# Performance work log

Measured on AMD Instinct MI355X. Metric: run time of the kernel, lower is better.

The kernel has to match this reference:

```python
import jax, jax.numpy as jnp
import numpy as np

B, C, V, L = 32, 32, 1024, 13  # batch, channels, nodes, seq_len
SUPPORT_LEN, ORDER = 3, 2
C_IN_TOTAL = (ORDER * SUPPORT_LEN + 1) * C  # 224
C_OUT = 64


def setup_inputs() -> dict:
    key = jax.random.key(0)
    ks = jax.random.split(key, 6)
    x = jax.random.normal(ks[0], (B, C, V, L), dtype=jnp.float32)
    # row-normalized random adjacencies (dense diffusion matrices)
    def adj(k):
        a = jax.random.uniform(k, (V, V), dtype=jnp.float32)
        return a / jnp.sum(a, axis=1, keepdims=True)
    A0, A1, A2 = adj(ks[1]), adj(ks[2]), adj(ks[3])
    W = jax.random.normal(ks[4], (C_OUT, C_IN_TOTAL), dtype=jnp.float32) * (1.0 / np.sqrt(C_IN_TOTAL))
    b = jnp.zeros((C_OUT,), dtype=jnp.float32)
    return {"x": x, "A0": A0, "A1": A1, "A2": A2, "W": W, "b": b}


def nconv(x, A):
    # x: [b, c, v, l], A: [v, w] -> [b, c, w, l]
    return jnp.einsum('bcvl,vw->bcwl', x, A)


def reference(x, A0, A1, A2, W, b):
    out = [x]
    for A in (A0, A1, A2):
        x1 = nconv(x, A)
        out.append(x1)
        for _ in range(2, ORDER + 1):
            x2 = nconv(x1, A)
            out.append(x2)
            x1 = x2
    h = jnp.concatenate(out, axis=1)  # [b, (order*support_len+1)*c, v, l]
    # 1x1 conv == channel contraction; dropout is identity in eval mode
    return jnp.einsum('bcvl,oc->bovl', h, W) + b[None, :, None, None]
```

## Files before the change

### kernel.cpp

```cpp
#include <hip/hip_runtime.h>
#include <hip/hip_bf16.h>
#include <cstdint>


#define SZE 13631488ull
#define OFF_AT  190840832ull
#define OFF_WB  197132288ull
#define WS_NEED 197160960ull

typedef __attribute__((ext_vector_type(8))) short short8;
typedef __attribute__((ext_vector_type(4))) float f32x4;

__device__ __forceinline__ unsigned short f2b(float f) {
    unsigned int u = __builtin_bit_cast(unsigned int, f);
    u += 0x7FFFu + ((u >> 16) & 1u);
    return (unsigned short)(u >> 16);
}

__device__ __forceinline__ void gl2lds16(const unsigned short* g, unsigned short* l) {
    __builtin_amdgcn_global_load_lds(
        (__attribute__((address_space(1))) void*)(g),
        (__attribute__((address_space(3))) void*)(l), 16, 0, 0);
}

__global__ __launch_bounds__(256) void k_prep_x(const float* __restrict__ x,
                                                unsigned short* __restrict__ T) {
    __shared__ unsigned short lb[13312];
    const int bc = blockIdx.x;
    const int b = bc >> 5, c = bc & 31;
    const int t = threadIdx.x;
    const float* xb = x + (size_t)bc * 13312;
    for (int k = 0; k < 13; ++k) {
        int i4 = k * 256 + t;
        float4 v = ((const float4*)xb)[i4];
        int e = i4 * 4;
        lb[e+0] = f2b(v.x); lb[e+1] = f2b(v.y); lb[e+2] = f2b(v.z); lb[e+3] = f2b(v.w);
    }
    __syncthreads();
    for (int l = 0; l < 13; ++l) {
        int v0 = t * 4;
        ushort4 val;
        val.x = lb[(v0+0)*13 + l];
        val.y = lb[(v0+1)*13 + l];
        val.z = lb[(v0+2)*13 + l];
        val.w = lb[(v0+3)*13 + l];
        *(ushort4*)(T + ((size_t)((b*13 + l)*32 + c) << 10) + v0) = val;
    }
}

__global__ __launch_bounds__(256) void k_prep_A(const float* __restrict__ A0,
                                                const float* __restrict__ A1,
                                                const float* __restrict__ A2,
                                                unsigned short* __restrict__ AT) {
    const float* A = blockIdx.z == 0 ? A0 : blockIdx.z == 1 ? A1 : A2;
    unsigned short* D = AT + (size_t)blockIdx.z * 1024 * 1024;
    __shared__ float tile[32][33];
    int v0 = blockIdx.y * 32, w0 = blockIdx.x * 32;
    int c = threadIdx.x & 31, r = threadIdx.x >> 5;
    for (int p = 0; p < 4; ++p) {
        int rr = r + p * 8;
        tile[rr][c] = A[(size_t)(v0 + rr) * 1024 + w0 + c];
    }
    __syncthreads();
    for (int p = 0; p < 4; ++p) {
        int rr = r + p * 8;
        D[(size_t)(w0 + rr) * 1024 + v0 + c] = f2b(tile[c][rr]);
    }
}

__global__ __launch_bounds__(256) void k_prep_W(const float* __restrict__ W,
                                                unsigned short* __restrict__ Wb) {
    int idx = blockIdx.x * 256 + threadIdx.x;
    Wb[idx] = f2b(W[idx]);
}

__global__ __launch_bounds__(256) void k_h0t(const unsigned short* __restrict__ T,
                                             unsigned short* __restrict__ Ht) {
    __shared__ unsigned short tb[416 * 64];
    const int b  = blockIdx.x >> 4;
    const int v0 = (blockIdx.x & 15) * 64;
    const int t  = threadIdx.x;
    const unsigned short* Tb = T + (size_t)b * 416 * 1024;
    for (int it = 0; it < 13; ++it) {
        int q = it * 256 + t;
        int row = q >> 3, seg = q & 7;
        *(uint4*)(tb + row * 64 + seg * 8) =
            *(const uint4*)(Tb + (size_t)row * 1024 + v0 + seg * 8);
    }
    __syncthreads();
    for (int it = 0; it < 4; ++it) {
        int p = it * 256 + t;
        if (p < 832) {
            int vi = p & 63, l = p >> 6;
            ushort4 pk[4];
#pragma unroll
            for (int j = 0; j < 4; ++j) {
                ushort4 u;
                u.x = tb[(l * 32 + j * 4 + 0) * 64 + vi];
                u.y = tb[(l * 32 + j * 4 + 1) * 64 + vi];
                u.z = tb[(l * 32 + j * 4 + 2) * 64 + vi];
                u.w = tb[(l * 32 + j * 4 + 3) * 64 + vi];
                pk[j] = u;
            }
            size_t m = (size_t)b * 13312 + (size_t)(v0 + vi) * 13 + l;
            unsigned short* dst = Ht + m * 224;
#pragma unroll
            for (int j = 0; j < 4; ++j) *(ushort4*)(dst + j * 4) = pk[j];
#pragma unroll
            for (int j = 0; j < 4; ++j) {
                ushort4 u;
                u.x = tb[(l * 32 + 16 + j * 4 + 0) * 64 + vi];
                u.y = tb[(l * 32 + 16 + j * 4 + 1) * 64 + vi];
                u.z = tb[(l * 32 + 16 + j * 4 + 2) * 64 + vi];
                u.w = tb[(l * 32 + 16 + j * 4 + 3) * 64 + vi];
                *(ushort4*)(dst + 16 + j * 4) = u;
            }
        }
    }
}

__global__ __launch_bounds__(256) void k_gemm(const unsigned short* __restrict__ Xb, long xz,
                                              const unsigned short* __restrict__ Pb,
                                              unsigned short* __restrict__ Tout, long tz,
                                              unsigned short* __restrict__ Ht, int cc0b,
                                              int doT) {
    __shared__ union {
        struct { unsigned short xs[4096]; unsigned short ps[4096]; } s;
        unsigned short cs[16384];
        unsigned short ct[128 * 136];
    } lds;
    const int z = blockIdx.z;
    const unsigned short* X = Xb + (size_t)z * (size_t)xz;
    const unsigned short* P = Pb + (size_t)z * (1024u * 1024u);
    const int i0 = blockIdx.x * 128;
    const int j0 = blockIdx.y * 128;
    const int t = threadIdx.x;
    const int lane = t & 63, wave = t >> 6;
    const int l16 = lane & 15, quad = lane >> 4;
    const int wi = (wave >> 1) * 64, wj = (wave & 1) * 64;

    f32x4 acc[4][4] = {};

    const int row = t >> 2, seg = t & 3;
    const unsigned short* xg0 = X + (size_t)(i0 + row) * 1024 + seg * 8;
    const unsigned short* xg1 = xg0 + (size_t)64 * 1024;
    const unsigned short* pg0 = P + (size_t)(j0 + row) * 1024 + seg * 8;
    const unsigned short* pg1 = pg0 + (size_t)64 * 1024;
    unsigned short* lx0 = lds.s.xs + t * 8;
    unsigned short* lx1 = lds.s.xs + 2048 + t * 8;
    unsigned short* lp0 = lds.s.ps + t * 8;
    unsigned short* lp1 = lds.s.ps + 2048 + t * 8;

    for (int kt = 0; kt < 32; ++kt) {
        const int ko = kt * 32;
        gl2lds16(xg0 + ko, lx0);
        gl2lds16(xg1 + ko, lx1);
        gl2lds16(pg0 + ko, lp0);
        gl2lds16(pg1 + ko, lp1);
        __syncthreads();
        short8 a[4], b[4];
#pragma unroll
        for (int mi = 0; mi < 4; ++mi)
            a[mi] = *(const short8*)(lds.s.xs + (wi + mi * 16 + l16) * 32 + quad * 8);
#pragma unroll
        for (int nj = 0; nj < 4; ++nj)
            b[nj] = *(const short8*)(lds.s.ps + (wj + nj * 16 + l16) * 32 + quad * 8);
#pragma unroll
        for (int mi = 0; mi < 4; ++mi)
#pragma unroll
            for (int nj = 0; nj < 4; ++nj)
                acc[mi][nj] = __builtin_amdgcn_mfma_f32_16x16x32_bf16(a[mi], b[nj], acc[mi][nj], 0, 0, 0);
        __syncthreads();
    }

    if (doT) {
#pragma unroll
        for (int mi = 0; mi < 4; ++mi)
#pragma unroll
            for (int nj = 0; nj < 4; ++nj)
#pragma unroll
                for (int r = 0; r < 4; ++r)
                    lds.cs[(wi + mi * 16 + quad * 4 + r) * 128 + (wj + nj * 16 + l16)] =
                        f2b(acc[mi][nj][r]);
        __syncthreads();
        unsigned short* O = Tout + (size_t)z * (size_t)tz;
#pragma unroll
        for (int rep = 0; rep < 8; ++rep) {
            int e0 = rep * 2048 + t * 8;
            int rr = e0 >> 7, cc = e0 & 127;
            *(uint4*)(O + (size_t)(i0 + rr) * 1024 + j0 + cc) = *(const uint4*)(lds.cs + e0);
        }
        __syncthreads();
    }

#pragma unroll
    for (int mi = 0; mi < 4; ++mi)
#pragma unroll
        for (int nj = 0; nj < 4; ++nj) {
            ushort4 pk;
            pk.x = f2b(acc[mi][nj][0]);
            pk.y = f2b(acc[mi][nj][1]);
            pk.z = f2b(acc[mi][nj][2]);
            pk.w = f2b(acc[mi][nj][3]);
            *(ushort4*)(lds.ct + (wj + nj * 16 + l16) * 136 + wi + mi * 16 + quad * 4) = pk;
        }
    __syncthreads();
    const int cc0 = cc0b + 64 * z;
#pragma unroll
    for (int it = 0; it < 8; ++it) {
        int q = it * 256 + t;
        int sg = q & 3, v = (q >> 2) & 127, s = q >> 9;
        int p = (i0 >> 5) + s;
        int b = p / 13, l = p - b * 13;
        size_t m = (size_t)b * 13312 + (size_t)(j0 + v) * 13 + l;
        *(uint4*)(Ht + m * 224 + cc0 + sg * 8) =
            *(const uint4*)(lds.ct + v * 136 + s * 32 + sg * 8);
    }
}

__global__ __launch_bounds__(256) void k_fc(const unsigned short* __restrict__ Ht,
                                            const unsigned short* __restrict__ Wb,
                                            const float* __restrict__ bias,
                                            float* __restrict__ y) {
    __shared__ union {
        struct { unsigned short w[64 * 232]; unsigned short a[208 * 40]; } s;
        float sy[64 * 212];
    } lds;
    const int bid = blockIdx.x;
    const int b = bid >> 6, v0 = (bid & 63) * 16;
    const size_t m0 = (size_t)b * 13312 + (size_t)v0 * 13;
    const int t = threadIdx.x;
    const int lane = t & 63, wave = t >> 6;
    const int l16 = lane & 15, quad = lane >> 4;
    const int o0 = wave * 16;

    for (int it = 0; it < 7; ++it) {
        int q = it * 256 + t;
        int o = q / 28, sg = q % 28;
        *(uint4*)(lds.s.w + o * 232 + sg * 8) = *(const uint4*)(Wb + o * 224 + sg * 8);
    }
    float bv = bias[o0 + l16];
    f32x4 acc[13];
#pragma unroll
    for (int mf = 0; mf < 13; ++mf) acc[mf] = (f32x4){bv, bv, bv, bv};

    for (int kk = 0; kk < 7; ++kk) {
        __syncthreads();
        for (int it = 0; it < 4; ++it) {
            int q = it * 256 + t;
            if (q < 832) {
                int r = q >> 2, sg = q & 3;
                *(uint4*)(lds.s.a + r * 40 + sg * 8) =
                    *(const uint4*)(Ht + (m0 + r) * 224 + kk * 32 + sg * 8);
            }
        }
        __syncthreads();
        short8 bf = *(const short8*)(lds.s.w + (o0 + l16) * 232 + kk * 32 + quad * 8);
#pragma unroll
        for (int mf = 0; mf < 13; ++mf) {
            short8 af = *(const short8*)(lds.s.a + (mf * 16 + l16) * 40 + quad * 8);
            acc[mf] = __builtin_amdgcn_mfma_f32_16x16x32_bf16(af, bf, acc[mf], 0, 0, 0);
        }
    }
    __syncthreads();
#pragma unroll
    for (int mf = 0; mf < 13; ++mf)
#pragma unroll
        for (int r = 0; r < 4; ++r)
            lds.sy[(o0 + l16) * 212 + mf * 16 + quad * 4 + r] = acc[mf][r];
    __syncthreads();
    float* yb = y + (size_t)b * 851968 + (size_t)v0 * 13;
    for (int it = 0; it < 13; ++it) {
        int q = it * 256 + t;
        int o = q / 52, sg = q % 52;
        *(float4*)(yb + (size_t)o * 13312 + sg * 4) = *(const float4*)(lds.sy + o * 212 + sg * 4);
    }
}

extern "C" void kernel_launch(void* const* d_in, const int* in_sizes, int n_in,
                              void* d_out, int out_size, void* d_ws, size_t ws_size,
                              hipStream_t stream) {
    const float* x    = (const float*)d_in[0];
    const float* A0   = (const float*)d_in[1];
    const float* A1   = (const float*)d_in[2];
    const float* A2   = (const float*)d_in[3];
    const float* W    = (const float*)d_in[4];
    const float* bias = (const float*)d_in[5];

    if (ws_size < WS_NEED) return;

    unsigned short* Ht = (unsigned short*)d_ws;
    unsigned short* AT = (unsigned short*)((char*)d_ws + OFF_AT);
    unsigned short* Wb = (unsigned short*)((char*)d_ws + OFF_WB);
    unsigned short* Tarena = (unsigned short*)d_out;

    k_prep_x<<<1024, 256, 0, stream>>>(x, Tarena);
    k_prep_A<<<dim3(32, 32, 3), 256, 0, stream>>>(A0, A1, A2, AT);
    k_prep_W<<<56, 256, 0, stream>>>(W, Wb);
    k_h0t<<<512, 256, 0, stream>>>(Tarena, Ht);
    k_gemm<<<dim3(104, 8, 3), 256, 0, stream>>>(Tarena, 0L, AT,
                                                Tarena + SZE, (long)SZE, Ht, 32, 1);
    k_gemm<<<dim3(104, 8, 3), 256, 0, stream>>>(Tarena + SZE, (long)SZE, AT,
                                                nullptr, 0L, Ht, 64, 0);
    k_fc<<<2048, 256, 0, stream>>>(Ht, Wb, bias, (float*)d_out);
}
```

Before: 551.0 us.

## Fuse x prep with H0 transpose, deepen GEMM K-tile, pad LDS, async loads in fc

Merges k_prep_x and k_h0t into one kernel that converts x to bf16 and writes both the transposed T layout and the first 32 channels of Ht from shared memory, dropping a launch and a global round trip. The diffusion GEMM now stages a K=64 tile per barrier pair instead of K=32, which halves the number of syncs at the cost of double the LDS footprint. The output staging tile is padded to 132 columns to reduce bank conflicts. The fc kernel loads activations with global_load_lds instead of going through registers, removing its row padding.

```diff
diff --git a/kernel.cpp b/kernel.cpp
--- a/kernel.cpp
+++ b/kernel.cpp
@@ -23,28 +23,44 @@
         (__attribute__((address_space(3))) void*)(l), 16, 0, 0);
 }
 
-__global__ __launch_bounds__(256) void k_prep_x(const float* __restrict__ x,
-                                                unsigned short* __restrict__ T) {
-    __shared__ unsigned short lb[13312];
-    const int bc = blockIdx.x;
-    const int b = bc >> 5, c = bc & 31;
+__global__ __launch_bounds__(256) void k_prep(const float* __restrict__ x,
+                                              unsigned short* __restrict__ T,
+                                              unsigned short* __restrict__ Ht) {
+    __shared__ unsigned short sb[32 * 840];
+    const int b = blockIdx.x >> 4, vc = blockIdx.x & 15;
     const int t = threadIdx.x;
-    const float* xb = x + (size_t)bc * 13312;
-    for (int k = 0; k < 13; ++k) {
-        int i4 = k * 256 + t;
-        float4 v = ((const float4*)xb)[i4];
-        int e = i4 * 4;
-        lb[e+0] = f2b(v.x); lb[e+1] = f2b(v.y); lb[e+2] = f2b(v.z); lb[e+3] = f2b(v.w);
-    }
-    __syncthreads();
-    for (int l = 0; l < 13; ++l) {
-        int v0 = t * 4;
-        ushort4 val;
-        val.x = lb[(v0+0)*13 + l];
-        val.y = lb[(v0+1)*13 + l];
-        val.z = lb[(v0+2)*13 + l];
-        val.w = lb[(v0+3)*13 + l];
-        *(ushort4*)(T + ((size_t)((b*13 + l)*32 + c) << 10) + v0) = val;
+    const float4* xb = (const float4*)x;
+    for (int it = 0; it < 26; ++it) {
+        int q = it * 256 + t;
+        int c = q / 208, f = q - c * 208;
+        float4 u = xb[(size_t)(b * 32 + c) * 3328 + vc * 208 + f];
+        ushort4 pk; pk.x = f2b(u.x); pk.y = f2b(u.y); pk.z = f2b(u.z); pk.w = f2b(u.w);
+        *(ushort4*)(sb + c * 840 + f * 4) = pk;
+    }
+    __syncthreads();
+    unsigned short* Tb = T + (size_t)b * 13 * 32 * 1024 + (size_t)vc * 64;
+    for (int it = 0; it < 26; ++it) {
+        int q = it * 256 + t;
+        int l = q >> 9, r = q & 511, c = r >> 4, sg = r & 15;
+        const unsigned short* src = sb + c * 840 + l;
+        ushort4 pk;
+        pk.x = src[(sg * 4 + 0) * 13];
+        pk.y = src[(sg * 4 + 1) * 13];
+        pk.z = src[(sg * 4 + 2) * 13];
+        pk.w = src[(sg * 4 + 3) * 13];
+        *(ushort4*)(Tb + (size_t)(l * 32 + c) * 1024 + sg * 4) = pk;
+    }
+    unsigned short* Hb = Ht + ((size_t)b * 13312 + (size_t)vc * 832) * 224;
+    for (int it = 0; it < 26; ++it) {
+        int q = it * 256 + t;
+        int v = q / 104, r = q - v * 104, l = r >> 3, cs = r & 7;
+        const unsigned short* src = sb + v * 13 + l;
+        ushort4 pk;
+        pk.x = src[(cs * 4 + 0) * 840];
+        pk.y = src[(cs * 4 + 1) * 840];
+        pk.z = src[(cs * 4 + 2) * 840];
+        pk.w = src[(cs * 4 + 3) * 840];
+        *(ushort4*)(Hb + (size_t)(v * 13 + l) * 224 + cs * 4) = pk;
     }
 }
 
@@ -74,59 +90,14 @@
     Wb[idx] = f2b(W[idx]);
 }
 
-__global__ __launch_bounds__(256) void k_h0t(const unsigned short* __restrict__ T,
-                                             unsigned short* __restrict__ Ht) {
-    __shared__ unsigned short tb[416 * 64];
-    const int b  = blockIdx.x >> 4;
-    const int v0 = (blockIdx.x & 15) * 64;
-    const int t  = threadIdx.x;
-    const unsigned short* Tb = T + (size_t)b * 416 * 1024;
-    for (int it = 0; it < 13; ++it) {
-        int q = it * 256 + t;
-        int row = q >> 3, seg = q & 7;
-        *(uint4*)(tb + row * 64 + seg * 8) =
-            *(const uint4*)(Tb + (size_t)row * 1024 + v0 + seg * 8);
-    }
-    __syncthreads();
-    for (int it = 0; it < 4; ++it) {
-        int p = it * 256 + t;
-        if (p < 832) {
-            int vi = p & 63, l = p >> 6;
-            ushort4 pk[4];
-#pragma unroll
-            for (int j = 0; j < 4; ++j) {
-                ushort4 u;
-                u.x = tb[(l * 32 + j * 4 + 0) * 64 + vi];
-                u.y = tb[(l * 32 + j * 4 + 1) * 64 + vi];
-                u.z = tb[(l * 32 + j * 4 + 2) * 64 + vi];
-                u.w = tb[(l * 32 + j * 4 + 3) * 64 + vi];
-                pk[j] = u;
-            }
-            size_t m = (size_t)b * 13312 + (size_t)(v0 + vi) * 13 + l;
-            unsigned short* dst = Ht + m * 224;
-#pragma unroll
-            for (int j = 0; j < 4; ++j) *(ushort4*)(dst + j * 4) = pk[j];
-#pragma unroll
-            for (int j = 0; j < 4; ++j) {
-                ushort4 u;
-                u.x = tb[(l * 32 + 16 + j * 4 + 0) * 64 + vi];
-                u.y = tb[(l * 32 + 16 + j * 4 + 1) * 64 + vi];
-                u.z = tb[(l * 32 + 16 + j * 4 + 2) * 64 + vi];
-                u.w = tb[(l * 32 + 16 + j * 4 + 3) * 64 + vi];
-                *(ushort4*)(dst + 16 + j * 4) = u;
-            }
-        }
-    }
-}
-
 __global__ __launch_bounds__(256) void k_gemm(const unsigned short* __restrict__ Xb, long xz,
                                               const unsigned short* __restrict__ Pb,
                                               unsigned short* __restrict__ Tout, long tz,
                                               unsigned short* __restrict__ Ht, int cc0b,
                                               int doT) {
     __shared__ union {
-        struct { unsigned short xs[4096]; unsigned short ps[4096]; } s;
-        unsigned short cs[16384];
+        struct { unsigned short xs[8192]; unsigned short ps[8192]; } s;
+        unsigned short cs[128 * 132];
         unsigned short ct[128 * 136];
     } lds;
     const int z = blockIdx.z;
@@ -147,48 +118,54 @@
     const unsigned short* pg0 = P + (size_t)(j0 + row) * 1024 + seg * 8;
     const unsigned short* pg1 = pg0 + (size_t)64 * 1024;
     unsigned short* lx0 = lds.s.xs + t * 8;
-    unsigned short* lx1 = lds.s.xs + 2048 + t * 8;
     unsigned short* lp0 = lds.s.ps + t * 8;
-    unsigned short* lp1 = lds.s.ps + 2048 + t * 8;
-
-    for (int kt = 0; kt < 32; ++kt) {
-        const int ko = kt * 32;
-        gl2lds16(xg0 + ko, lx0);
-        gl2lds16(xg1 + ko, lx1);
-        gl2lds16(pg0 + ko, lp0);
-        gl2lds16(pg1 + ko, lp1);
-        __syncthreads();
-        short8 a[4], b[4];
+
+    for (int kt = 0; kt < 16; ++kt) {
+        const int ko = kt * 64;
+        gl2lds16(xg0 + ko,      lx0);
+        gl2lds16(xg1 + ko,      lx0 + 2048);
+        gl2lds16(xg0 + ko + 32, lx0 + 4096);
+        gl2lds16(xg1 + ko + 32, lx0 + 6144);
+        gl2lds16(pg0 + ko,      lp0);
+        gl2lds16(pg1 + ko,      lp0 + 2048);
+        gl2lds16(pg0 + ko + 32, lp0 + 4096);
+        gl2lds16(pg1 + ko + 32, lp0 + 6144);
+        __syncthreads();
+#pragma unroll
+        for (int p = 0; p < 2; ++p) {
+            short8 a[4], b[4];
+#pragma unroll
+            for (int mi = 0; mi < 4; ++mi)
+                a[mi] = *(const short8*)(lds.s.xs + p * 4096 + (wi + mi * 16 + l16) * 32 + quad * 8);
+#pragma unroll
+            for (int nj = 0; nj < 4; ++nj)
+                b[nj] = *(const short8*)(lds.s.ps + p * 4096 + (wj + nj * 16 + l16) * 32 + quad * 8);
+#pragma unroll
+            for (int mi = 0; mi < 4; ++mi)
+#pragma unroll
+                for (int nj = 0; nj < 4; ++nj)
+                    acc[mi][nj] = __builtin_amdgcn_mfma_f32_16x16x32_bf16(a[mi], b[nj], acc[mi][nj], 0, 0, 0);
+        }
+        __syncthreads();
+    }
+
+    if (doT) {
 #pragma unroll
         for (int mi = 0; mi < 4; ++mi)
-            a[mi] = *(const short8*)(lds.s.xs + (wi + mi * 16 + l16) * 32 + quad * 8);
-#pragma unroll
-        for (int nj = 0; nj < 4; ++nj)
-            b[nj] = *(const short8*)(lds.s.ps + (wj + nj * 16 + l16) * 32 + quad * 8);
-#pragma unroll
-        for (int mi = 0; mi < 4; ++mi)
 #pragma unroll
             for (int nj = 0; nj < 4; ++nj)
-                acc[mi][nj] = __builtin_amdgcn_mfma_f32_16x16x32_bf16(a[mi], b[nj], acc[mi][nj], 0, 0, 0);
-        __syncthreads();
-    }
-
-    if (doT) {
-#pragma unroll
-        for (int mi = 0; mi < 4; ++mi)
-#pragma unroll
-            for (int nj = 0; nj < 4; ++nj)
 #pragma unroll
                 for (int r = 0; r < 4; ++r)
-                    lds.cs[(wi + mi * 16 + quad * 4 + r) * 128 + (wj + nj * 16 + l16)] =
+                    lds.cs[(wi + mi * 16 + quad * 4 + r) * 132 + (wj + nj * 16 + l16)] =
                         f2b(acc[mi][nj][r]);
         __syncthreads();
         unsigned short* O = Tout + (size_t)z * (size_t)tz;
 #pragma unroll
         for (int rep = 0; rep < 8; ++rep) {
-            int e0 = rep * 2048 + t * 8;
-            int rr = e0 >> 7, cc = e0 & 127;
-            *(uint4*)(O + (size_t)(i0 + rr) * 1024 + j0 + cc) = *(const uint4*)(lds.cs + e0);
+            int q = rep * 256 + t;
+            int rr = q >> 4, sg = q & 15;
+            *(uint4*)(O + (size_t)(i0 + rr) * 1024 + j0 + sg * 8) =
+                *(const uint4*)(lds.cs + rr * 132 + sg * 8);
         }
         __syncthreads();
     }
@@ -223,7 +200,7 @@
                                             const float* __restrict__ bias,
                                             float* __restrict__ y) {
     __shared__ union {
-        struct { unsigned short w[64 * 232]; unsigned short a[208 * 40]; } s;
+        struct { unsigned short w[64 * 232]; unsigned short a[208 * 32]; } s;
         float sy[64 * 212];
     } lds;
     const int bid = blockIdx.x;
@@ -248,17 +225,15 @@
         __syncthreads();
         for (int it = 0; it < 4; ++it) {
             int q = it * 256 + t;
-            if (q < 832) {
-                int r = q >> 2, sg = q & 3;
-                *(uint4*)(lds.s.a + r * 40 + sg * 8) =
-                    *(const uint4*)(Ht + (m0 + r) * 224 + kk * 32 + sg * 8);
-            }
+            if (q < 832)
+                gl2lds16(Ht + (m0 + (q >> 2)) * 224 + kk * 32 + (q & 3) * 8,
+                         lds.s.a + q * 8);
         }
         __syncthreads();
         short8 bf = *(const short8*)(lds.s.w + (o0 + l16) * 232 + kk * 32 + quad * 8);
 #pragma unroll
         for (int mf = 0; mf < 13; ++mf) {
-            short8 af = *(const short8*)(lds.s.a + (mf * 16 + l16) * 40 + quad * 8);
+            short8 af = *(const short8*)(lds.s.a + (mf * 16 + l16) * 32 + quad * 8);
             acc[mf] = __builtin_amdgcn_mfma_f32_16x16x32_bf16(af, bf, acc[mf], 0, 0, 0);
         }
     }
@@ -294,10 +269,9 @@
     unsigned short* Wb = (unsigned short*)((char*)d_ws + OFF_WB);
     unsigned short* Tarena = (unsigned short*)d_out;
 
-    k_prep_x<<<1024, 256, 0, stream>>>(x, Tarena);
+    k_prep<<<512, 256, 0, stream>>>(x, Tarena, Ht);
     k_prep_A<<<dim3(32, 32, 3), 256, 0, stream>>>(A0, A1, A2, AT);
     k_prep_W<<<56, 256, 0, stream>>>(W, Wb);
-    k_h0t<<<512, 256, 0, stream>>>(Tarena, Ht);
     k_gemm<<<dim3(104, 8, 3), 256, 0, stream>>>(Tarena, 0L, AT,
                                                 Tarena + SZE, (long)SZE, Ht, 32, 1);
     k_gemm<<<dim3(104, 8, 3), 256, 0, stream>>>(Tarena + SZE, (long)SZE, AT,
```

Result: faster. 511.0 us (-7.3%).
